# Performance work log

Measured on AMD Instinct MI355X. Metric: run time of the kernel, lower is better.

The kernel has to match this reference:

```python
import jax, jax.numpy as jnp
import numpy as np

TEMPERATURE = 0.5
EPS = 1e-8  # torch CosineSimilarity eps


def setup_inputs() -> dict:
    key = jax.random.key(0)
    k1, k2 = jax.random.split(key)
    B, D = 4096, 256
    return {
        "z_i": jax.random.normal(k1, (B, D), dtype=jnp.float32),
        "z_j": jax.random.normal(k2, (B, D), dtype=jnp.float32),
    }


def reference(z_i, z_j):
    B = z_i.shape[0]
    N = 2 * B
    z = jnp.concatenate([z_i, z_j], axis=0)  # [N, D]
    # cosine similarity == normalized dot product (eps-clamped norms like torch)
    norms = jnp.maximum(jnp.linalg.norm(z, axis=1, keepdims=True), EPS)
    zn = z / norms
    sim = jnp.matmul(zn, zn.T) / TEMPERATURE  # [N, N]

    idx = jnp.arange(B)
    # positives: diag(sim, +B) and diag(sim, -B)
    pos = jnp.concatenate([sim[idx, idx + B], sim[idx + B, idx]])  # [N]

    # CrossEntropy with label 0 over [pos_i, negatives_i] reduces to
    # logsumexp over row i excluding the self-diagonal, minus pos_i.
    r = jnp.arange(N)
    neg_inf = jnp.finfo(sim.dtype).min
    sim_masked = jnp.where(r[:, None] == r[None, :], neg_inf, sim)
    lse = jax.nn.logsumexp(sim_masked, axis=1)  # [N]

    loss = (jnp.sum(lse) - jnp.sum(pos)) / N
    return loss
```

## Files before the change

kernel.cpp:

```cpp
#include <hip/hip_runtime.h>
#include <cstdint>

#define B_ROWS 4096
#define N_ROWS 8192
#define D_DIM  256
#define BT     128
#define TGRID  64
#define NTILES 2080
#define NKT    4

typedef __attribute__((ext_vector_type(4))) float f32x4;
typedef __attribute__((ext_vector_type(2))) unsigned long u64x2;

__device__ __forceinline__ void gload16(const void* g, void* l) {
    __builtin_amdgcn_global_load_lds(
        (const __attribute__((address_space(1))) void*)g,
        (__attribute__((address_space(3))) void*)l, 16, 0, 0);
}

__device__ __forceinline__ f32x4 exp4(f32x4 v) {
    f32x4 r;
    r.x = __expf(v.x); r.y = __expf(v.y); r.z = __expf(v.z); r.w = __expf(v.w);
    return r;
}

__device__ __forceinline__ unsigned f2e4m3(float f) {
    union { float f; unsigned u; } v; v.f = f;
    unsigned s = (v.u >> 24) & 0x80u;
    unsigned mag = v.u & 0x7fffffffu;
    int e = (int)(mag >> 23) - 127;
    if (e >= -6) {
        unsigned r = mag + 0x7ffffu + ((mag >> 20) & 1u);
        int e2 = (int)(r >> 23) - 127;
        unsigned m3 = (r >> 20) & 7u;
        return s | (unsigned)((e2 + 7) << 3) | m3;
    }
    if (e < -10) return s;
    float q = rintf(fabsf(f) * 512.0f);
    unsigned qi = (unsigned)q;
    return s | qi;
}

__global__ __launch_bounds__(256) void normpos_kernel(const float* __restrict__ zi,
                                                      const float* __restrict__ zj,
                                                      unsigned char* __restrict__ zn,
                                                      float* __restrict__ pospartial) {
    int wid = threadIdx.x >> 6;
    int lane = threadIdx.x & 63;
    int p = blockIdx.x * 4 + wid;
    f32x4 ga = *(const f32x4*)(zi + (size_t)p * D_DIM + lane * 4);
    f32x4 gb = *(const f32x4*)(zj + (size_t)p * D_DIM + lane * 4);
    float sa = ga.x * ga.x + ga.y * ga.y + ga.z * ga.z + ga.w * ga.w;
    float sb = gb.x * gb.x + gb.y * gb.y + gb.z * gb.z + gb.w * gb.w;
    #pragma unroll
    for (int m = 1; m < 64; m <<= 1) { sa += __shfl_xor(sa, m, 64); sb += __shfl_xor(sb, m, 64); }
    float fa = 1.41421356237309515f / fmaxf(sqrtf(sa), 1e-8f);
    float fb = 1.41421356237309515f / fmaxf(sqrtf(sb), 1e-8f);
    f32x4 na, nb;
    na.x = ga.x * fa; na.y = ga.y * fa; na.z = ga.z * fa; na.w = ga.w * fa;
    nb.x = gb.x * fb; nb.y = gb.y * fb; nb.z = gb.z * fb; nb.w = gb.w * fb;
    unsigned pa = f2e4m3(na.x) | (f2e4m3(na.y) << 8) | (f2e4m3(na.z) << 16) | (f2e4m3(na.w) << 24);
    unsigned pb = f2e4m3(nb.x) | (f2e4m3(nb.y) << 8) | (f2e4m3(nb.z) << 16) | (f2e4m3(nb.w) << 24);
    int bytepos = (lane >> 4) * 64 + ((lane >> 1) & 3) * 16 + ((lane >> 3) & 1) * 8 + 4 * (lane & 1);
    *(unsigned*)(zn + (size_t)p * 256 + bytepos) = pa;
    *(unsigned*)(zn + (size_t)(p + B_ROWS) * 256 + bytepos) = pb;
    float d = na.x * nb.x + na.y * nb.y + na.z * nb.z + na.w * nb.w;
    #pragma unroll
    for (int m = 1; m < 64; m <<= 1) d += __shfl_xor(d, m, 64);
    if (lane == 0) pospartial[p] = d;
}

__global__ __launch_bounds__(256, 3) void simclr_gemm_kernel(const unsigned char* __restrict__ zn,
                                                             float* __restrict__ P) {
    __shared__ unsigned char As[BT * 64];
    __shared__ unsigned char Bs[BT * 64];
    __shared__ float rPpart[2][BT];
    __shared__ float cPpart[2][BT];

    const int tid = threadIdx.x;
    const int lane = tid & 63, wid = tid >> 6;
    const int wr = wid >> 1, wc = wid & 1;

    int bid = (int)((blockIdx.x & 7) * (NTILES / 8) + (blockIdx.x >> 3));
    int ti = (int)((129.0f - sqrtf(16641.0f - 8.0f * (float)bid)) * 0.5f);
    while ((ti + 1) * TGRID - ((ti + 1) * ti) / 2 <= bid) ++ti;
    while (ti * TGRID - (ti * (ti - 1)) / 2 > bid) --ti;
    const int tj = ti + (bid - (ti * TGRID - (ti * (ti - 1)) / 2));

    const char* gA = (const char*)zn + (size_t)ti * BT * 256;
    const char* gB = (const char*)zn + (size_t)tj * BT * 256;

    const int r0 = tid >> 2;
    const int sch = (tid & 3) ^ ((tid >> 3) & 3);
    const size_t gof0 = (size_t)r0 * 256 + (size_t)sch * 16;
    const size_t gof1 = (size_t)(64 + r0) * 256 + (size_t)sch * 16;
    const unsigned lo0 = (unsigned)tid * 16;
    const unsigned lo1 = 4096u + (unsigned)tid * 16;

    f32x4 acc[4][4];
    #pragma unroll
    for (int m = 0; m < 4; ++m)
        #pragma unroll
        for (int n = 0; n < 4; ++n)
            acc[m][n] = (f32x4){0.f, 0.f, 0.f, 0.f};

    const int ysw = (lane >> 4) ^ (((lane & 15) >> 1) & 3);
    const int arow = wr * 64 + (lane & 15);
    const int brow = wc * 64 + (lane & 15);

    #pragma unroll
    for (int kt = 0; kt < NKT; ++kt) {
        const size_t kb = (size_t)kt * 64;
        gload16(gA + gof0 + kb, &As[lo0]);
        gload16(gA + gof1 + kb, &As[lo1]);
        gload16(gB + gof0 + kb, &Bs[lo0]);
        gload16(gB + gof1 + kb, &Bs[lo1]);
        __syncthreads();

        u64x2 af[4], bfr[4];
        #pragma unroll
        for (int m = 0; m < 4; ++m)
            af[m] = *(const u64x2*)&As[(arow + m * 16) * 64 + ysw * 16];
        #pragma unroll
        for (int n = 0; n < 4; ++n)
            bfr[n] = *(const u64x2*)&Bs[(brow + n * 16) * 64 + ysw * 16];

        #pragma unroll
        for (int m = 0; m < 4; ++m)
            #pragma unroll
            for (int n = 0; n < 4; ++n) {
                acc[m][n] = __builtin_amdgcn_mfma_f32_16x16x32_fp8_fp8(
                    (long)af[m].x, (long)bfr[n].x, acc[m][n], 0, 0, 0);
                acc[m][n] = __builtin_amdgcn_mfma_f32_16x16x32_fp8_fp8(
                    (long)af[m].y, (long)bfr[n].y, acc[m][n], 0, 0, 0);
            }
        __syncthreads();
    }

    float cs[4] = {0.f, 0.f, 0.f, 0.f};
    #pragma unroll
    for (int m = 0; m < 4; ++m) {
        f32x4 ef[4];
        #pragma unroll
        for (int n = 0; n < 4; ++n) ef[n] = exp4(acc[m][n]);
        f32x4 rv = ef[0] + ef[1] + ef[2] + ef[3];
        #pragma unroll
        for (int msk = 1; msk <= 8; msk <<= 1) {
            rv.x += __shfl_xor(rv.x, msk, 64);
            rv.y += __shfl_xor(rv.y, msk, 64);
            rv.z += __shfl_xor(rv.z, msk, 64);
            rv.w += __shfl_xor(rv.w, msk, 64);
        }
        if ((lane & 15) == 0) {
            int rbase = wr * 64 + m * 16 + (lane >> 4) * 4;
            rPpart[wc][rbase + 0] = rv.x;
            rPpart[wc][rbase + 1] = rv.y;
            rPpart[wc][rbase + 2] = rv.z;
            rPpart[wc][rbase + 3] = rv.w;
        }
        #pragma unroll
        for (int n = 0; n < 4; ++n)
            cs[n] += ef[n].x + ef[n].y + ef[n].z + ef[n].w;
    }
    #pragma unroll
    for (int n = 0; n < 4; ++n) {
        float c = cs[n];
        c += __shfl_xor(c, 16, 64);
        c += __shfl_xor(c, 32, 64);
        if (lane < 16) cPpart[wr][wc * 64 + n * 16 + lane] = c;
    }
    __syncthreads();

    if (tid < BT) {
        P[(size_t)tj * N_ROWS + ti * BT + tid] = rPpart[0][tid] + rPpart[1][tid];
    } else if (ti != tj) {
        int t = tid - BT;
        P[(size_t)ti * N_ROWS + tj * BT + t] = cPpart[0][t] + cPpart[1][t];
    }
}

__global__ __launch_bounds__(256) void reduce_rows_kernel(const float* __restrict__ P,
                                                          const float* __restrict__ pospartial,
                                                          float* __restrict__ blockpart) {
    const float E2 = 7.38905609893065f;
    int row = blockIdx.x * 256 + threadIdx.x;
    float s = 0.f;
    #pragma unroll 16
    for (int src = 0; src < TGRID; ++src)
        s += P[(size_t)src * N_ROWS + row];
    float v = logf(s - E2);
    if (threadIdx.x < 128)
        v -= 2.0f * pospartial[blockIdx.x * 128 + threadIdx.x];
    #pragma unroll
    for (int m = 1; m < 64; m <<= 1) v += __shfl_xor(v, m, 64);
    __shared__ float ws[4];
    if ((threadIdx.x & 63) == 0) ws[threadIdx.x >> 6] = v;
    __syncthreads();
    if (threadIdx.x == 0) blockpart[blockIdx.x] = ws[0] + ws[1] + ws[2] + ws[3];
}

__global__ __launch_bounds__(64) void final_kernel(const float* __restrict__ blockpart,
                                                   float* __restrict__ out) {
    int lane = threadIdx.x;
    float v = (lane < 32) ? blockpart[lane] : 0.f;
    #pragma unroll
    for (int m = 1; m < 64; m <<= 1) v += __shfl_xor(v, m, 64);
    if (lane == 0) out[0] = v / (float)N_ROWS;
}

extern "C" void kernel_launch(void* const* d_in, const int* in_sizes, int n_in,
                              void* d_out, int out_size, void* d_ws, size_t ws_size,
                              hipStream_t stream) {
    const float* zi = (const float*)d_in[0];
    const float* zj = (const float*)d_in[1];
    char* ws = (char*)d_ws;
    unsigned char* zn = (unsigned char*)ws;
    float* P = (float*)(ws + 2 * 1024 * 1024);
    float* pospartial = (float*)(ws + 4 * 1024 * 1024);
    float* blockpart = (float*)(ws + 4 * 1024 * 1024 + 16 * 1024);

    normpos_kernel<<<B_ROWS / 4, 256, 0, stream>>>(zi, zj, zn, pospartial);
    simclr_gemm_kernel<<<NTILES, 256, 0, stream>>>(zn, P);
    reduce_rows_kernel<<<N_ROWS / 256, 256, 0, stream>>>(P, pospartial, blockpart);
    final_kernel<<<1, 64, 0, stream>>>(blockpart, (float*)d_out);
}
```

Before: 38.24 us.

## Load full K-depth tiles into LDS upfront instead of per-k-step loads

```diff
diff --git a/kernel.cpp b/kernel.cpp
--- a/kernel.cpp
+++ b/kernel.cpp
@@ -7,7 +7,6 @@
 #define BT     128
 #define TGRID  64
 #define NTILES 2080
-#define NKT    4
 
 typedef __attribute__((ext_vector_type(4))) float f32x4;
 typedef __attribute__((ext_vector_type(2))) unsigned long u64x2;
@@ -70,10 +69,10 @@
     if (lane == 0) pospartial[p] = d;
 }
 
-__global__ __launch_bounds__(256, 3) void simclr_gemm_kernel(const unsigned char* __restrict__ zn,
+__global__ __launch_bounds__(256, 2) void simclr_gemm_kernel(const unsigned char* __restrict__ zn,
                                                              float* __restrict__ P) {
-    __shared__ unsigned char As[BT * 64];
-    __shared__ unsigned char Bs[BT * 64];
+    __shared__ unsigned char As[4 * 8192];
+    __shared__ unsigned char Bs[4 * 8192];
     __shared__ float rPpart[2][BT];
     __shared__ float cPpart[2][BT];
 
@@ -92,10 +91,17 @@
 
     const int r0 = tid >> 2;
     const int sch = (tid & 3) ^ ((tid >> 3) & 3);
-    const size_t gof0 = (size_t)r0 * 256 + (size_t)sch * 16;
-    const size_t gof1 = (size_t)(64 + r0) * 256 + (size_t)sch * 16;
-    const unsigned lo0 = (unsigned)tid * 16;
-    const unsigned lo1 = 4096u + (unsigned)tid * 16;
+    const unsigned lo = (unsigned)tid * 16;
+
+    #pragma unroll
+    for (int g = 0; g < 4; ++g) {
+        #pragma unroll
+        for (int h = 0; h < 2; ++h) {
+            size_t go = (size_t)(h * 64 + r0) * 256 + (size_t)g * 64 + (size_t)sch * 16;
+            gload16(gA + go, &As[g * 8192 + h * 4096 + lo]);
+            gload16(gB + go, &Bs[g * 8192 + h * 4096 + lo]);
+        }
+    }
 
     f32x4 acc[4][4];
     #pragma unroll
@@ -108,23 +114,17 @@
     const int arow = wr * 64 + (lane & 15);
     const int brow = wc * 64 + (lane & 15);
 
-    #pragma unroll
-    for (int kt = 0; kt < NKT; ++kt) {
-        const size_t kb = (size_t)kt * 64;
-        gload16(gA + gof0 + kb, &As[lo0]);
-        gload16(gA + gof1 + kb, &As[lo1]);
-        gload16(gB + gof0 + kb, &Bs[lo0]);
-        gload16(gB + gof1 + kb, &Bs[lo1]);
-        __syncthreads();
-
+    __syncthreads();
+
+    #pragma unroll
+    for (int g = 0; g < 4; ++g) {
         u64x2 af[4], bfr[4];
         #pragma unroll
         for (int m = 0; m < 4; ++m)
-            af[m] = *(const u64x2*)&As[(arow + m * 16) * 64 + ysw * 16];
+            af[m] = *(const u64x2*)&As[g * 8192 + (arow + m * 16) * 64 + ysw * 16];
         #pragma unroll
         for (int n = 0; n < 4; ++n)
-            bfr[n] = *(const u64x2*)&Bs[(brow + n * 16) * 64 + ysw * 16];
-
+            bfr[n] = *(const u64x2*)&Bs[g * 8192 + (brow + n * 16) * 64 + ysw * 16];
         #pragma unroll
         for (int m = 0; m < 4; ++m)
             #pragma unroll
@@ -134,7 +134,6 @@
                 acc[m][n] = __builtin_amdgcn_mfma_f32_16x16x32_fp8_fp8(
                     (long)af[m].y, (long)bfr[n].y, acc[m][n], 0, 0, 0);
             }
-        __syncthreads();
     }
 
     float cs[4] = {0.f, 0.f, 0.f, 0.f};
```

New measurement: 40.95 us. 1.07x slower.

## Make GEMM persistent over multiple tiles with double-buffered LDS prefetch

Applied to the files above, without the earlier changes.

```diff
diff --git a/kernel.cpp b/kernel.cpp
--- a/kernel.cpp
+++ b/kernel.cpp
@@ -7,7 +7,7 @@
 #define BT     128
 #define TGRID  64
 #define NTILES 2080
-#define NKT    4
+#define NPB    512
 
 typedef __attribute__((ext_vector_type(4))) float f32x4;
 typedef __attribute__((ext_vector_type(2))) unsigned long u64x2;
@@ -70,10 +70,10 @@
     if (lane == 0) pospartial[p] = d;
 }
 
-__global__ __launch_bounds__(256, 3) void simclr_gemm_kernel(const unsigned char* __restrict__ zn,
+__global__ __launch_bounds__(256, 2) void simclr_gemm_kernel(const unsigned char* __restrict__ zn,
                                                              float* __restrict__ P) {
-    __shared__ unsigned char As[BT * 64];
-    __shared__ unsigned char Bs[BT * 64];
+    __shared__ unsigned char As[2][8192];
+    __shared__ unsigned char Bs[2][8192];
     __shared__ float rPpart[2][BT];
     __shared__ float cPpart[2][BT];
 
@@ -81,14 +81,8 @@
     const int lane = tid & 63, wid = tid >> 6;
     const int wr = wid >> 1, wc = wid & 1;
 
-    int bid = (int)((blockIdx.x & 7) * (NTILES / 8) + (blockIdx.x >> 3));
-    int ti = (int)((129.0f - sqrtf(16641.0f - 8.0f * (float)bid)) * 0.5f);
-    while ((ti + 1) * TGRID - ((ti + 1) * ti) / 2 <= bid) ++ti;
-    while (ti * TGRID - (ti * (ti - 1)) / 2 > bid) --ti;
-    const int tj = ti + (bid - (ti * TGRID - (ti * (ti - 1)) / 2));
-
-    const char* gA = (const char*)zn + (size_t)ti * BT * 256;
-    const char* gB = (const char*)zn + (size_t)tj * BT * 256;
+    const int xb = (int)((blockIdx.x & 7) * (NPB / 8) + (blockIdx.x >> 3));
+    const int nt = 4 + ((xb & 15) == 0 ? 1 : 0);
 
     const int r0 = tid >> 2;
     const int sch = (tid & 3) ^ ((tid >> 3) & 3);
@@ -97,86 +91,122 @@
     const unsigned lo0 = (unsigned)tid * 16;
     const unsigned lo1 = 4096u + (unsigned)tid * 16;
 
-    f32x4 acc[4][4];
-    #pragma unroll
-    for (int m = 0; m < 4; ++m)
-        #pragma unroll
-        for (int n = 0; n < 4; ++n)
-            acc[m][n] = (f32x4){0.f, 0.f, 0.f, 0.f};
-
     const int ysw = (lane >> 4) ^ (((lane & 15) >> 1) & 3);
     const int arow = wr * 64 + (lane & 15);
     const int brow = wc * 64 + (lane & 15);
 
-    #pragma unroll
-    for (int kt = 0; kt < NKT; ++kt) {
-        const size_t kb = (size_t)kt * 64;
-        gload16(gA + gof0 + kb, &As[lo0]);
-        gload16(gA + gof1 + kb, &As[lo1]);
-        gload16(gB + gof0 + kb, &Bs[lo0]);
-        gload16(gB + gof1 + kb, &Bs[lo1]);
+#define TILE_OF(r_)  (((r_) < 4) ? (xb + ((r_) << 9)) : (2048 + (xb >> 4)))
+#define DECODE(t_, ti_, tj_) do {                                              \
+    int a_ = (int)((129.0f - sqrtf(16641.0f - 8.0f * (float)(t_))) * 0.5f);    \
+    while ((a_ + 1) * TGRID - ((a_ + 1) * a_) / 2 <= (t_)) ++a_;               \
+    while (a_ * TGRID - (a_ * (a_ - 1)) / 2 > (t_)) --a_;                      \
+    (ti_) = a_; (tj_) = a_ + ((t_) - (a_ * TGRID - (a_ * (a_ - 1)) / 2));      \
+} while (0)
+#define STAGE(buf_, gA_, gB_, kt_) do {                                        \
+    size_t kb_ = (size_t)(kt_) * 64;                                           \
+    gload16((gA_) + gof0 + kb_, &As[buf_][lo0]);                               \
+    gload16((gA_) + gof1 + kb_, &As[buf_][lo1]);                               \
+    gload16((gB_) + gof0 + kb_, &Bs[buf_][lo0]);                               \
+    gload16((gB_) + gof1 + kb_, &Bs[buf_][lo1]);                               \
+} while (0)
+
+    int ti, tj, ti_n, tj_n;
+    DECODE(TILE_OF(0), ti, tj);
+    const char* gAc = (const char*)zn + (size_t)ti * BT * 256;
+    const char* gBc = (const char*)zn + (size_t)tj * BT * 256;
+    const char* gAn = gAc;
+    const char* gBn = gBc;
+    const int S = 4 * nt;
+
+    STAGE(0, gAc, gBc, 0);
+
+    for (int r = 0; r < nt; ++r) {
+        f32x4 acc[4][4];
+        #pragma unroll
+        for (int m = 0; m < 4; ++m)
+            #pragma unroll
+            for (int n = 0; n < 4; ++n)
+                acc[m][n] = (f32x4){0.f, 0.f, 0.f, 0.f};
+
+        #pragma unroll
+        for (int kt = 0; kt < 4; ++kt) {
+            const int s = 4 * r + kt;
+            __syncthreads();
+            if (s + 1 < S) {
+                const int kt2 = (s + 1) & 3;
+                if (kt2 == 0) {
+                    DECODE(TILE_OF(r + 1), ti_n, tj_n);
+                    gAn = (const char*)zn + (size_t)ti_n * BT * 256;
+                    gBn = (const char*)zn + (size_t)tj_n * BT * 256;
+                    STAGE((s + 1) & 1, gAn, gBn, 0);
+                } else {
+                    STAGE((s + 1) & 1, gAc, gBc, kt2);
+                }
+            }
+            u64x2 af[4], bfr[4];
+            #pragma unroll
+            for (int m = 0; m < 4; ++m)
+                af[m] = *(const u64x2*)&As[s & 1][(arow + m * 16) * 64 + ysw * 16];
+            #pragma unroll
+            for (int n = 0; n < 4; ++n)
+                bfr[n] = *(const u64x2*)&Bs[s & 1][(brow + n * 16) * 64 + ysw * 16];
+            #pragma unroll
+            for (int m = 0; m < 4; ++m)
+                #pragma unroll
+                for (int n = 0; n < 4; ++n) {
+                    acc[m][n] = __builtin_amdgcn_mfma_f32_16x16x32_fp8_fp8(
+                        (long)af[m].x, (long)bfr[n].x, acc[m][n], 0, 0, 0);
+                    acc[m][n] = __builtin_amdgcn_mfma_f32_16x16x32_fp8_fp8(
+                        (long)af[m].y, (long)bfr[n].y, acc[m][n], 0, 0, 0);
+                }
+        }
+
+        float cs[4] = {0.f, 0.f, 0.f, 0.f};
+        #pragma unroll
+        for (int m = 0; m < 4; ++m) {
+            f32x4 ef[4];
+            #pragma unroll
+            for (int n = 0; n < 4; ++n) ef[n] = exp4(acc[m][n]);
+            f32x4 rv = ef[0] + ef[1] + ef[2] + ef[3];
+            #pragma unroll
+            for (int msk = 1; msk <= 8; msk <<= 1) {
+                rv.x += __shfl_xor(rv.x, msk, 64);
+                rv.y += __shfl_xor(rv.y, msk, 64);
+                rv.z += __shfl_xor(rv.z, msk, 64);
+                rv.w += __shfl_xor(rv.w, msk, 64);
+            }
+            if ((lane & 15) == 0) {
+                int rbase = wr * 64 + m * 16 + (lane >> 4) * 4;
+                rPpart[wc][rbase + 0] = rv.x;
+                rPpart[wc][rbase + 1] = rv.y;
+                rPpart[wc][rbase + 2] = rv.z;
+                rPpart[wc][rbase + 3] = rv.w;
+            }
+            #pragma unroll
+            for (int n = 0; n < 4; ++n)
+                cs[n] += ef[n].x + ef[n].y + ef[n].z + ef[n].w;
+        }
+        #pragma unroll
+        for (int n = 0; n < 4; ++n) {
+            float c = cs[n];
+            c += __shfl_xor(c, 16, 64);
+            c += __shfl_xor(c, 32, 64);
+            if (lane < 16) cPpart[wr][wc * 64 + n * 16 + lane] = c;
+        }
         __syncthreads();
 
-        u64x2 af[4], bfr[4];
-        #pragma unroll
-        for (int m = 0; m < 4; ++m)
-            af[m] = *(const u64x2*)&As[(arow + m * 16) * 64 + ysw * 16];
-        #pragma unroll
-        for (int n = 0; n < 4; ++n)
-            bfr[n] = *(const u64x2*)&Bs[(brow + n * 16) * 64 + ysw * 16];
-
-        #pragma unroll
-        for (int m = 0; m < 4; ++m)
-            #pragma unroll
-            for (int n = 0; n < 4; ++n) {
-                acc[m][n] = __builtin_amdgcn_mfma_f32_16x16x32_fp8_fp8(
-                    (long)af[m].x, (long)bfr[n].x, acc[m][n], 0, 0, 0);
-                acc[m][n] = __builtin_amdgcn_mfma_f32_16x16x32_fp8_fp8(
-                    (long)af[m].y, (long)bfr[n].y, acc[m][n], 0, 0, 0);
-            }
-        __syncthreads();
+        if (tid < BT) {
+            P[(size_t)tj * N_ROWS + ti * BT + tid] = rPpart[0][tid] + rPpart[1][tid];
+        } else if (ti != tj) {
+            int t = tid - BT;
+            P[(size_t)ti * N_ROWS + tj * BT + t] = cPpart[0][t] + cPpart[1][t];
+        }
+
+        ti = ti_n; tj = tj_n; gAc = gAn; gBc = gBn;
     }
-
-    float cs[4] = {0.f, 0.f, 0.f, 0.f};
-    #pragma unroll
-    for (int m = 0; m < 4; ++m) {
-        f32x4 ef[4];
-        #pragma unroll
-        for (int n = 0; n < 4; ++n) ef[n] = exp4(acc[m][n]);
-        f32x4 rv = ef[0] + ef[1] + ef[2] + ef[3];
-        #pragma unroll
-        for (int msk = 1; msk <= 8; msk <<= 1) {
-            rv.x += __shfl_xor(rv.x, msk, 64);
-            rv.y += __shfl_xor(rv.y, msk, 64);
-            rv.z += __shfl_xor(rv.z, msk, 64);
-            rv.w += __shfl_xor(rv.w, msk, 64);
-        }
-        if ((lane & 15) == 0) {
-            int rbase = wr * 64 + m * 16 + (lane >> 4) * 4;
-            rPpart[wc][rbase + 0] = rv.x;
-            rPpart[wc][rbase + 1] = rv.y;
-            rPpart[wc][rbase + 2] = rv.z;
-            rPpart[wc][rbase + 3] = rv.w;
-        }
-        #pragma unroll
-        for (int n = 0; n < 4; ++n)
-            cs[n] += ef[n].x + ef[n].y + ef[n].z + ef[n].w;
-    }
-    #pragma unroll
-    for (int n = 0; n < 4; ++n) {
-        float c = cs[n];
-        c += __shfl_xor(c, 16, 64);
-        c += __shfl_xor(c, 32, 64);
-        if (lane < 16) cPpart[wr][wc * 64 + n * 16 + lane] = c;
-    }
-    __syncthreads();
-
-    if (tid < BT) {
-        P[(size_t)tj * N_ROWS + ti * BT + tid] = rPpart[0][tid] + rPpart[1][tid];
-    } else if (ti != tj) {
-        int t = tid - BT;
-        P[(size_t)ti * N_ROWS + tj * BT + t] = cPpart[0][t] + cPpart[1][t];
-    }
+#undef STAGE
+#undef DECODE
+#undef TILE_OF
 }
 
 __global__ __launch_bounds__(256) void reduce_rows_kernel(const float* __restrict__ P,
@@ -220,7 +250,7 @@
     float* blockpart = (float*)(ws + 4 * 1024 * 1024 + 16 * 1024);
 
     normpos_kernel<<<B_ROWS / 4, 256, 0, stream>>>(zi, zj, zn, pospartial);
-    simclr_gemm_kernel<<<NTILES, 256, 0, stream>>>(zn, P);
+    simclr_gemm_kernel<<<NPB, 256, 0, stream>>>(zn, P);
     reduce_rows_kernel<<<N_ROWS / 256, 256, 0, stream>>>(P, pospartial, blockpart);
     final_kernel<<<1, 64, 0, stream>>>(blockpart, (float*)d_out);
 }
```

Result: slower. 45.36 us (+18.6%).
